# Kernel optimization log

Hardware: AMD Instinct MI355X
Metric: run time of the kernel (lower is better)

## Reference

```python
import jax, jax.numpy as jnp
import numpy as np

H = 32      # query heads
HK = 8      # kv heads
HD = 64     # head dim
D = 2048    # model dim
BASE = 10000.0
NEG = -1e9


def _rope_cos_sin(L):
    inv_freq = 1.0 / (BASE ** (jnp.arange(0, HD, 2, dtype=jnp.float32) / HD))  # [HD/2]
    freqs = jnp.arange(L, dtype=jnp.float32)[:, None] * inv_freq[None, :]       # [L, HD/2]
    emb = jnp.concatenate([freqs, freqs], axis=-1)                               # [L, HD]
    return jnp.cos(emb), jnp.sin(emb)


def _rotate_half(x):
    x1, x2 = jnp.split(x, 2, axis=-1)
    return jnp.concatenate([-x2, x1], axis=-1)


def setup_inputs() -> dict:
    key = jax.random.key(0)
    ks = jax.random.split(key, 5)
    B, L = 2, 2048
    x = jax.random.normal(ks[0], (B, L, D), dtype=jnp.float32)
    Wq = jax.random.normal(ks[1], (D, D), dtype=jnp.float32) * 0.02
    Wk = jax.random.normal(ks[2], (HK * HD, D), dtype=jnp.float32) * 0.02
    Wv = jax.random.normal(ks[3], (HK * HD, D), dtype=jnp.float32) * 0.02
    Wo = jax.random.normal(ks[4], (D, D), dtype=jnp.float32) * 0.02
    causal = jnp.where(jnp.tril(jnp.ones((L, L), dtype=bool)), 0.0, NEG)
    mask = causal[None, None].astype(jnp.float32)  # [1,1,L,L] additive mask
    return {"x": x, "Wq": Wq, "Wk": Wk, "Wv": Wv, "Wo": Wo, "mask": mask}


def reference(x, Wq, Wk, Wv, Wo, mask):
    B, L, _ = x.shape
    # projections (nn.Linear: y = x @ W^T), split heads -> [B, heads, L, HD]
    q = jnp.einsum('bld,ed->ble', x, Wq).reshape(B, L, H, HD).transpose(0, 2, 1, 3)
    k = jnp.einsum('bld,ed->ble', x, Wk).reshape(B, L, HK, HD).transpose(0, 2, 1, 3)
    v = jnp.einsum('bld,ed->ble', x, Wv).reshape(B, L, HK, HD).transpose(0, 2, 1, 3)
    # RoPE (plain branch: L <= original_max); cos/sin [L,HD] broadcast over B,heads
    cos, sin = _rope_cos_sin(L)
    q = q * cos + _rotate_half(q) * sin
    k = k * cos + _rotate_half(k) * sin
    # GQA: repeat_interleave kv heads to H heads
    rep = H // HK
    k = jnp.repeat(k, rep, axis=1)  # [B,H,L,HD]
    v = jnp.repeat(v, rep, axis=1)
    scores = jnp.einsum('bhld,bhmd->bhlm', q, k) / np.float32(np.sqrt(HD)) + mask
    attn = jax.nn.softmax(scores, axis=-1)
    out = jnp.einsum('bhlm,bhmd->blhd', attn, v).reshape(B, L, D)
    return jnp.einsum('ble,de->bld', out, Wo)
```

## Files before the change

kernel.cpp:

```cpp
#include <hip/hip_runtime.h>
#include <math.h>

#define NH 32
#define NHK 8
#define HD 64
#define DMODEL 2048
#define LSEQ 2048
#define NB 2
#define QKV_N 3072

typedef __attribute__((ext_vector_type(8))) short short8;
typedef __attribute__((ext_vector_type(4))) float floatx4;

__device__ __forceinline__ unsigned short f2bf(float f) {
  unsigned u = __float_as_uint(f);
  return (unsigned short)((u + 0x7FFFu + ((u >> 16) & 1u)) >> 16);
}
__device__ __forceinline__ float bf2f(unsigned short v) {
  return __uint_as_float((unsigned)v << 16);
}
__device__ __forceinline__ float fast_exp2(float x) {
#if __has_builtin(__builtin_amdgcn_exp2f)
  return __builtin_amdgcn_exp2f(x);
#else
  return __expf(x * 0.69314718f);
#endif
}
__device__ __forceinline__ unsigned pack_bf_trunc(float hi, float lo) {
  return __builtin_amdgcn_perm(__float_as_uint(hi), __float_as_uint(lo), 0x07060302u);
}
__device__ __forceinline__ void stage16g(const char* g_lane,
                                         unsigned short* lds_wave_base, int lane) {
#if __has_builtin(__builtin_amdgcn_global_load_lds)
  __builtin_amdgcn_global_load_lds(
      (const __attribute__((address_space(1))) void*)(g_lane),
      (__attribute__((address_space(3))) void*)(lds_wave_base), 16, 0, 0);
#else
  *(uint4*)(lds_wave_base + lane * 8) = *(const uint4*)g_lane;
#endif
}

__global__ __launch_bounds__(256) void rope_tab(float2* __restrict__ tab) {
  int i = blockIdx.x * 256 + threadIdx.x;
  int d = i & 31, l = i >> 5;
  float invf = (float)pow(10000.0, -(double)d / 32.0);
  float ang = (float)l * invf;
  double sd, cd;
  sincos((double)ang, &sd, &cd);
  tab[i] = make_float2((float)cd, (float)sd);
}

__global__ __launch_bounds__(256) void cvt_bf16(const float* __restrict__ src,
                                                unsigned short* __restrict__ dst,
                                                int n4) {
  int i = blockIdx.x * 256 + threadIdx.x;
  if (i >= n4) return;
  float4 v = ((const float4*)src)[i];
  ushort4 o;
  o.x = f2bf(v.x); o.y = f2bf(v.y); o.z = f2bf(v.z); o.w = f2bf(v.w);
  ((ushort4*)dst)[i] = o;
}

__global__ __launch_bounds__(256) void cvt_w3(const float* __restrict__ Wq,
                                              const float* __restrict__ Wk,
                                              const float* __restrict__ Wv,
                                              unsigned short* __restrict__ dst) {
  const int NQ = DMODEL * DMODEL / 4, NK = 512 * DMODEL / 4;
  int i = blockIdx.x * 256 + threadIdx.x;
  const float* src;
  int off;
  if (i < NQ) { src = Wq; off = i; }
  else if (i < NQ + NK) { src = Wk; off = i - NQ; }
  else { src = Wv; off = i - NQ - NK; }
  float4 v = ((const float4*)src)[off];
  ushort4 o;
  o.x = f2bf(v.x); o.y = f2bf(v.y); o.z = f2bf(v.z); o.w = f2bf(v.w);
  ((ushort4*)dst)[i] = o;
}

template <int BN, bool BF16C>
__global__ __launch_bounds__(512, 2) void gemm8(const unsigned short* __restrict__ A,
                                                const unsigned short* __restrict__ B,
                                                void* __restrict__ Cv, int K, int ldc) {
  constexpr int CN = BN / 64;
  constexpr int BUFB = BN * 32;
  __shared__ unsigned short As[4 * 256 * 32];
  __shared__ unsigned short Bs[4 * BUFB];

  const int tid = threadIdx.x;
  const int wave = tid >> 6, lane = tid & 63;
  const int quad = lane >> 4, l16 = lane & 15;
  const int wm = wave & 1, wn = wave >> 1;

  const int nwg = gridDim.x * gridDim.y;
  const int orig = blockIdx.y * gridDim.x + blockIdx.x;
  const int swz = (orig & 7) * (nwg >> 3) + (orig >> 3);
  const int bx = swz % gridDim.x, by = swz / gridDim.x;
  const int m0 = by * 256, n0 = bx * BN;

  const int kt = K >> 5;

  const int sgrow = wave * 16 + (lane >> 2);
  const int cchunk = (lane & 3) ^ ((lane >> 3) & 3);
  const char* AgB = (const char*)(A + (size_t)(m0 + sgrow) * K + cchunk * 8);
  const char* BgB = (const char*)(B + (size_t)(n0 + sgrow) * K + cchunk * 8);

  auto stageA = [&](int t2) {
    unsigned short* dst = &As[((t2 & 3) << 13) + wave * 512];
#pragma unroll
    for (int u = 0; u < 2; ++u)
      stage16g(AgB + ((size_t)u * 128 * K + (size_t)t2 * 32) * 2, dst + u * 4096, lane);
  };
  auto stageB = [&](int t2) {
    unsigned short* dst = &Bs[(t2 & 3) * BUFB + wave * 512];
#pragma unroll
    for (int u = 0; u < BN / 128; ++u)
      stage16g(BgB + ((size_t)u * 128 * K + (size_t)t2 * 32) * 2, dst + u * 4096, lane);
  };

  const int sw8 = (quad ^ ((l16 >> 1) & 3)) * 8;

  floatx4 acc[8][CN] = {};

  stageA(0); stageB(0);
  stageA(1); stageB(1);
  stageA(2); stageB(2);

#pragma unroll 1
  for (int t = 0; t < kt; ++t) {
    if (t + 2 < kt) {
      if constexpr (BN == 256) asm volatile("s_waitcnt vmcnt(8)" ::: "memory");
      else                     asm volatile("s_waitcnt vmcnt(6)" ::: "memory");
    } else if (t + 1 < kt) {
      if constexpr (BN == 256) asm volatile("s_waitcnt vmcnt(4)" ::: "memory");
      else                     asm volatile("s_waitcnt vmcnt(3)" ::: "memory");
    } else {
      asm volatile("s_waitcnt vmcnt(0)" ::: "memory");
    }
    __builtin_amdgcn_s_barrier();
    __builtin_amdgcn_sched_barrier(0);

    const unsigned short* Asb = &As[(t & 3) << 13];
    const unsigned short* Bsb = &Bs[(t & 3) * BUFB];
    const unsigned short* Arow = Asb + (wm * 128 + l16) * 32 + sw8;
    const unsigned short* Brow = Bsb + (wn * 16 * CN + l16) * 32 + sw8;

    short8 bfr[CN], af[4];
#pragma unroll
    for (int j = 0; j < CN; ++j) bfr[j] = *(const short8*)(Brow + j * 16 * 32);
#pragma unroll
    for (int i = 0; i < 4; ++i) af[i] = *(const short8*)(Arow + i * 16 * 32);

    if (t + 3 < kt) stageA(t + 3);

    __builtin_amdgcn_s_setprio(1);
#pragma unroll
    for (int i = 0; i < 4; ++i)
#pragma unroll
      for (int j = 0; j < CN; ++j)
        acc[i][j] = __builtin_amdgcn_mfma_f32_16x16x32_bf16(af[i], bfr[j], acc[i][j], 0, 0, 0);
    __builtin_amdgcn_s_setprio(0);

#pragma unroll
    for (int i = 0; i < 4; ++i) af[i] = *(const short8*)(Arow + (64 + i * 16) * 32);

    if (t + 3 < kt) stageB(t + 3);

    __builtin_amdgcn_s_setprio(1);
#pragma unroll
    for (int i = 0; i < 4; ++i)
#pragma unroll
      for (int j = 0; j < CN; ++j)
        acc[4 + i][j] = __builtin_amdgcn_mfma_f32_16x16x32_bf16(af[i], bfr[j], acc[4 + i][j], 0, 0, 0);
    __builtin_amdgcn_s_setprio(0);
  }

#pragma unroll
  for (int i = 0; i < 8; ++i)
#pragma unroll
    for (int j = 0; j < CN; ++j)
#pragma unroll
      for (int r = 0; r < 4; ++r) {
        size_t idx = (size_t)(m0 + wm * 128 + i * 16 + quad * 4 + r) * ldc +
                     n0 + wn * 16 * CN + j * 16 + l16;
        if (BF16C)
          ((unsigned short*)Cv)[idx] = f2bf(acc[i][j][r]);
        else
          ((float*)Cv)[idx] = acc[i][j][r];
      }
}

__global__ __launch_bounds__(256) void ropek_cvt2(const unsigned short* __restrict__ qkvb,
                                                  const float2* __restrict__ tab,
                                                  unsigned short* __restrict__ kb) {
  int t = blockIdx.x * 256 + threadIdx.x;
  int d = t & 31;
  int rest = t >> 5;
  int khead = rest & 7;
  int bl = rest >> 3;
  int l = bl & (LSEQ - 1);
  int b = bl >> 11;
  const unsigned short* src = qkvb + (size_t)bl * QKV_N + DMODEL + khead * HD;
  float2 cs = tab[(size_t)l * 32 + d];
  float x1 = bf2f(src[d]), x2 = bf2f(src[d + 32]);
  unsigned short* dst = kb + ((size_t)((b * NHK + khead) * LSEQ + l)) * HD;
  dst[d] = f2bf(x1 * cs.x - x2 * cs.y);
  dst[d + 32] = f2bf(x2 * cs.x + x1 * cs.y);
}

__global__ __launch_bounds__(256) void vt_cvt2(const unsigned short* __restrict__ qkvb,
                                               unsigned short* __restrict__ vtb) {
  __shared__ unsigned short Lt[64][72];
  const int tt = blockIdx.x, kh = blockIdx.y, b = blockIdx.z;
  const int tid = threadIdx.x;
  const unsigned short* src =
      qkvb + ((size_t)(b * LSEQ + tt * 64)) * QKV_N + DMODEL + 512 + kh * HD;
  {
    int row = tid >> 2, c0 = (tid & 3) * 16;
    *(uint4*)&Lt[row][c0] = *(const uint4*)(src + (size_t)row * QKV_N + c0);
    *(uint4*)&Lt[row][c0 + 8] = *(const uint4*)(src + (size_t)row * QKV_N + c0 + 8);
  }
  __syncthreads();
  {
    int d = tid >> 2, seg = tid & 3;
    unsigned short o[16];
#pragma unroll
    for (int k = 0; k < 16; ++k) o[k] = Lt[seg * 16 + k][d];
    unsigned short* dst =
        vtb + ((size_t)((b * NHK + kh) * 80 + d)) * LSEQ + tt * 64 + seg * 16;
    *(uint4*)dst = *(uint4*)o;
    *(uint4*)(dst + 8) = *(uint4*)(o + 8);
  }
  if (tid < 64)
    vtb[((size_t)((b * NHK + kh) * 80 + 64)) * LSEQ + tt * 64 + tid] = 0x3F80;
}

__global__ __launch_bounds__(256, 3) void attn8(const unsigned short* __restrict__ qkvb,
                                                const float2* __restrict__ tab,
                                                const unsigned short* __restrict__ kb,
                                                const unsigned short* __restrict__ vtb,
                                                unsigned short* __restrict__ out) {
  const int kh = blockIdx.x;
  const int p = 63 - blockIdx.y;
  const int b = blockIdx.z;
  const int wave = threadIdx.x >> 6, lane = threadIdx.x & 63;
  const int quad = lane >> 4, l16 = lane & 15;
  const int h = kh * 4 + wave;

  __shared__ unsigned short Kbuf[2][64 * 64];
  __shared__ unsigned short Vbuf[2][72 * 64];
  __shared__ unsigned short Ps_all[4][32][72];
  unsigned short(*Ps)[72] = Ps_all[wave];

  const char* kbaseB = (const char*)(kb + ((size_t)(b * NHK + kh) * LSEQ) * HD);
  const char* vbaseB = (const char*)(vtb + ((size_t)(b * NHK + kh) * 80) * LSEQ);
  const float QSCALE = 0.125f * 1.44269504f;

  short8 qf[2][2];
  floatx4 O[2][5];

  auto loadQ = [&](int qb) {
#pragma unroll
    for (int i = 0; i < 2; ++i) {
      const int tok = qb + i * 16 + l16;
      const unsigned short* qr =
          qkvb + ((size_t)(b * LSEQ + tok)) * QKV_N + h * HD + quad * 8;
      uint4 lo = *(const uint4*)qr;
      uint4 hi = *(const uint4*)(qr + 32);
      const float2* tr = tab + (size_t)tok * 32 + quad * 8;
      float4 cs01 = ((const float4*)tr)[0];
      float4 cs23 = ((const float4*)tr)[1];
      float4 cs45 = ((const float4*)tr)[2];
      float4 cs67 = ((const float4*)tr)[3];
      float cosv[8] = {cs01.x, cs01.z, cs23.x, cs23.z, cs45.x, cs45.z, cs67.x, cs67.z};
      float sinv[8] = {cs01.y, cs01.w, cs23.y, cs23.w, cs45.y, cs45.w, cs67.y, cs67.w};
      const unsigned short* plo = (const unsigned short*)&lo;
      const unsigned short* phi = (const unsigned short*)&hi;
      unsigned short olo[8], ohi[8];
#pragma unroll
      for (int j = 0; j < 8; ++j) {
        float x1 = bf2f(plo[j]), x2 = bf2f(phi[j]);
        olo[j] = f2bf((x1 * cosv[j] - x2 * sinv[j]) * QSCALE);
        ohi[j] = f2bf((x2 * cosv[j] + x1 * sinv[j]) * QSCALE);
      }
      qf[i][0] = *(const short8*)olo;
      qf[i][1] = *(const short8*)ohi;
    }
  };
  auto zeroO = [&]() {
#pragma unroll
    for (int i = 0; i < 2; ++i)
#pragma unroll
      for (int j = 0; j < 5; ++j) O[i][j] = (floatx4){0.f, 0.f, 0.f, 0.f};
  };
  auto epilogue = [&](int qb) {
#pragma unroll
    for (int i = 0; i < 2; ++i) {
      float lv = __shfl(O[i][4][0], l16);
      float inv = 1.0f / lv;
      const size_t obase =
          ((size_t)(b * LSEQ + qb + i * 16 + l16)) * DMODEL + h * HD;
#pragma unroll
      for (int j = 0; j < 4; ++j) {
        uint2 w;
        w.x = (unsigned)f2bf(O[i][j][0] * inv) | ((unsigned)f2bf(O[i][j][1] * inv) << 16);
        w.y = (unsigned)f2bf(O[i][j][2] * inv) | ((unsigned)f2bf(O[i][j][3] * inv) << 16);
        *(uint2*)&out[obase + j * 16 + quad * 4] = w;
      }
    }
  };
  auto stageKV = [&](int bi, int kt) {
    unsigned short* Kd = Kbuf[bi];
    unsigned short* Vd = Vbuf[bi];
#pragma unroll
    for (int c = wave; c < 17; c += 4) {
      if (c < 8) {
        int o = c * 1024 + lane * 16;
        int row = o >> 7;
        int lgc = ((o >> 4) & 7) ^ (row & 7);
        stage16g(kbaseB + (size_t)(kt * 64 + row) * 128 + lgc * 16,
                 Kd + c * 512, lane);
      } else {
        int o = (c - 8) * 1024 + lane * 16;
        int row = o >> 7;
        int lgc = ((o >> 4) & 7) ^ (row & 7);
        stage16g(vbaseB + (size_t)row * (LSEQ * 2) + (size_t)kt * 128 + lgc * 16,
                 Vd + (c - 8) * 512, lane);
      }
    }
  };

  const int qb = p * 32;
  const int last = p >> 1;
  const int N = last + 1;

  loadQ(qb);
  zeroO();
  stageKV(0, 0);

#pragma unroll 1
  for (int m = 0; m < N; ++m) {
    __syncthreads();

    if (m + 1 < N) stageKV((m + 1) & 1, m + 1);

    const int kt = m;
    const unsigned short* Ks = Kbuf[m & 1];
    const unsigned short* Vs = Vbuf[m & 1];

    short8 kf[4][2];
#pragma unroll
    for (int t = 0; t < 4; ++t)
#pragma unroll
      for (int hf = 0; hf < 2; ++hf) {
        int row = t * 16 + l16;
        int phys = (4 * hf + quad) ^ (row & 7);
        kf[t][hf] = *(const short8*)&Ks[row * 64 + phys * 8];
      }

    floatx4 st[4][2];
#pragma unroll
    for (int t = 0; t < 4; ++t)
#pragma unroll
      for (int i = 0; i < 2; ++i) {
        floatx4 z = {0.f, 0.f, 0.f, 0.f};
        z = __builtin_amdgcn_mfma_f32_16x16x32_bf16(kf[t][0], qf[i][0], z, 0, 0, 0);
        st[t][i] = __builtin_amdgcn_mfma_f32_16x16x32_bf16(kf[t][1], qf[i][1], z, 0, 0, 0);
      }

    if (kt == last) {
      const int kofs = kt * 64 - qb;
#pragma unroll
      for (int t = 0; t < 4; ++t) {
        const int krow = kofs + 16 * t + quad * 4;
#pragma unroll
        for (int i = 0; i < 2; ++i) {
          const int qcol = 16 * i + l16;
          float sv[4];
#pragma unroll
          for (int r = 0; r < 4; ++r) {
            float v = st[t][i][r];
            if (krow + r > qcol) v = -1e30f;
            sv[r] = fast_exp2(v);
          }
          uint2 w;
          w.x = pack_bf_trunc(sv[1], sv[0]);
          w.y = pack_bf_trunc(sv[3], sv[2]);
          *(uint2*)&Ps[16 * i + l16][16 * t + quad * 4] = w;
        }
      }
    } else {
#pragma unroll
      for (int t = 0; t < 4; ++t)
#pragma unroll
        for (int i = 0; i < 2; ++i) {
          float sv[4];
#pragma unroll
          for (int r = 0; r < 4; ++r) sv[r] = fast_exp2(st[t][i][r]);
          uint2 w;
          w.x = pack_bf_trunc(sv[1], sv[0]);
          w.y = pack_bf_trunc(sv[3], sv[2]);
          *(uint2*)&Ps[16 * i + l16][16 * t + quad * 4] = w;
        }
    }

    short8 pf[2][2];
#pragma unroll
    for (int i = 0; i < 2; ++i)
#pragma unroll
      for (int hh = 0; hh < 2; ++hh)
        pf[i][hh] = *(const short8*)&Ps[16 * i + l16][32 * hh + quad * 8];
#pragma unroll
    for (int j = 0; j < 5; ++j) {
      int row = (j == 4) ? (64 + (l16 & 7)) : (j * 16 + l16);
      short8 vf0 = *(const short8*)&Vs[row * 64 + ((quad ^ (row & 7)) * 8)];
      short8 vf1 = *(const short8*)&Vs[row * 64 + (((4 + quad) ^ (row & 7)) * 8)];
#pragma unroll
      for (int i = 0; i < 2; ++i) {
        O[i][j] = __builtin_amdgcn_mfma_f32_16x16x32_bf16(vf0, pf[i][0], O[i][j], 0, 0, 0);
        O[i][j] = __builtin_amdgcn_mfma_f32_16x16x32_bf16(vf1, pf[i][1], O[i][j], 0, 0, 0);
      }
    }
  }

  epilogue(qb);
}

extern "C" void kernel_launch(void* const* d_in, const int* in_sizes, int n_in,
                              void* d_out, int out_size, void* d_ws,
                              size_t ws_size, hipStream_t stream) {
  const float* x = (const float*)d_in[0];
  const float* Wq = (const float*)d_in[1];
  const float* Wk = (const float*)d_in[2];
  const float* Wv = (const float*)d_in[3];
  const float* Wo = (const float*)d_in[4];
  float* out = (float*)d_out;

  char* ws = (char*)d_ws;
  unsigned short* qkvb = (unsigned short*)ws;
  float2* tab = (float2*)(ws + 25165824);
  unsigned short* kbuf = (unsigned short*)(ws + 25690112);
  unsigned short* vtb = (unsigned short*)(ws + 29884416);
  unsigned short* xb = (unsigned short*)(ws + 35127296);
  unsigned short* wqkvb = (unsigned short*)(ws + 51904512);
  unsigned short* aob = xb;
  unsigned short* wob = wqkvb;

  const int M = NB * LSEQ;
  dim3 blk(256);

  rope_tab<<<(LSEQ * 32) / 256, blk, 0, stream>>>(tab);
  cvt_bf16<<<(M * DMODEL / 4 + 255) / 256, blk, 0, stream>>>(x, xb, M * DMODEL / 4);
  cvt_w3<<<(QKV_N * DMODEL / 4) / 256, blk, 0, stream>>>(Wq, Wk, Wv, wqkvb);

  gemm8<256, true><<<dim3(QKV_N / 256, M / 256), dim3(512), 0, stream>>>(
      xb, wqkvb, qkvb, DMODEL, QKV_N);

  ropek_cvt2<<<(NB * LSEQ * 8 * 32) / 256, blk, 0, stream>>>(qkvb, tab, kbuf);
  vt_cvt2<<<dim3(LSEQ / 64, NHK, NB), blk, 0, stream>>>(qkvb, vtb);

  attn8<<<dim3(NHK, 64, NB), blk, 0, stream>>>(qkvb, tab, kbuf, vtb, aob);

  cvt_bf16<<<(DMODEL * DMODEL / 4 + 255) / 256, blk, 0, stream>>>(Wo, wob, DMODEL * DMODEL / 4);

  gemm8<128, false><<<dim3(DMODEL / 128, M / 256), dim3(512), 0, stream>>>(
      aob, wob, out, DMODEL, DMODEL);
}
```

Measured before the change: 303.6 us.

## Merge prep and mid kernels, add phased barrier schedule to QKV GEMM

The RoPE table, x conversion and Wq/Wk/Wv conversion now run as a single prep kernel. K-RoPE, the V transpose and the Wo conversion are merged into a single mid kernel. Together these cut the launch count from nine to five and remove the small-kernel tail gaps. The QKV GEMM also gains a PHASED variant that adds workgroup barriers and lgkmcnt waits around each MFMA phase to keep waves in lockstep. Those extra barriers could cost stall time, and the mid kernel's shared-memory allocation now applies to every block.

```diff
diff --git a/kernel.cpp b/kernel.cpp
--- a/kernel.cpp
+++ b/kernel.cpp
@@ -40,45 +40,47 @@
 #endif
 }
 
-__global__ __launch_bounds__(256) void rope_tab(float2* __restrict__ tab) {
-  int i = blockIdx.x * 256 + threadIdx.x;
-  int d = i & 31, l = i >> 5;
-  float invf = (float)pow(10000.0, -(double)d / 32.0);
-  float ang = (float)l * invf;
-  double sd, cd;
-  sincos((double)ang, &sd, &cd);
-  tab[i] = make_float2((float)cd, (float)sd);
-}
-
-__global__ __launch_bounds__(256) void cvt_bf16(const float* __restrict__ src,
-                                                unsigned short* __restrict__ dst,
-                                                int n4) {
-  int i = blockIdx.x * 256 + threadIdx.x;
-  if (i >= n4) return;
-  float4 v = ((const float4*)src)[i];
-  ushort4 o;
-  o.x = f2bf(v.x); o.y = f2bf(v.y); o.z = f2bf(v.z); o.w = f2bf(v.w);
-  ((ushort4*)dst)[i] = o;
-}
-
-__global__ __launch_bounds__(256) void cvt_w3(const float* __restrict__ Wq,
-                                              const float* __restrict__ Wk,
-                                              const float* __restrict__ Wv,
-                                              unsigned short* __restrict__ dst) {
+__global__ __launch_bounds__(256) void prep(const float* __restrict__ x,
+                                            const float* __restrict__ Wq,
+                                            const float* __restrict__ Wk,
+                                            const float* __restrict__ Wv,
+                                            float2* __restrict__ tab,
+                                            unsigned short* __restrict__ xb,
+                                            unsigned short* __restrict__ wqkvb) {
+  const int NTAB = LSEQ * 32;
+  const int NX = NB * LSEQ * DMODEL / 4;
+  int idx = blockIdx.x * 256 + threadIdx.x;
+  if (idx < NTAB) {
+    int d = idx & 31, l = idx >> 5;
+    float invf = (float)pow(10000.0, -(double)d / 32.0);
+    float ang = (float)l * invf;
+    double sd, cd;
+    sincos((double)ang, &sd, &cd);
+    tab[idx] = make_float2((float)cd, (float)sd);
+    return;
+  }
+  idx -= NTAB;
+  if (idx < NX) {
+    float4 v = ((const float4*)x)[idx];
+    ushort4 o;
+    o.x = f2bf(v.x); o.y = f2bf(v.y); o.z = f2bf(v.z); o.w = f2bf(v.w);
+    ((ushort4*)xb)[idx] = o;
+    return;
+  }
+  idx -= NX;
   const int NQ = DMODEL * DMODEL / 4, NK = 512 * DMODEL / 4;
-  int i = blockIdx.x * 256 + threadIdx.x;
   const float* src;
   int off;
-  if (i < NQ) { src = Wq; off = i; }
-  else if (i < NQ + NK) { src = Wk; off = i - NQ; }
-  else { src = Wv; off = i - NQ - NK; }
+  if (idx < NQ) { src = Wq; off = idx; }
+  else if (idx < NQ + NK) { src = Wk; off = idx - NQ; }
+  else { src = Wv; off = idx - NQ - NK; }
   float4 v = ((const float4*)src)[off];
   ushort4 o;
   o.x = f2bf(v.x); o.y = f2bf(v.y); o.z = f2bf(v.z); o.w = f2bf(v.w);
-  ((ushort4*)dst)[i] = o;
-}
-
-template <int BN, bool BF16C>
+  ((ushort4*)wqkvb)[idx] = o;
+}
+
+template <int BN, bool BF16C, bool PHASED>
 __global__ __launch_bounds__(512, 2) void gemm8(const unsigned short* __restrict__ A,
                                                 const unsigned short* __restrict__ B,
                                                 void* __restrict__ Cv, int K, int ldc) {
@@ -146,33 +148,71 @@
     const unsigned short* Brow = Bsb + (wn * 16 * CN + l16) * 32 + sw8;
 
     short8 bfr[CN], af[4];
-#pragma unroll
-    for (int j = 0; j < CN; ++j) bfr[j] = *(const short8*)(Brow + j * 16 * 32);
-#pragma unroll
-    for (int i = 0; i < 4; ++i) af[i] = *(const short8*)(Arow + i * 16 * 32);
-
-    if (t + 3 < kt) stageA(t + 3);
-
-    __builtin_amdgcn_s_setprio(1);
-#pragma unroll
-    for (int i = 0; i < 4; ++i)
-#pragma unroll
-      for (int j = 0; j < CN; ++j)
-        acc[i][j] = __builtin_amdgcn_mfma_f32_16x16x32_bf16(af[i], bfr[j], acc[i][j], 0, 0, 0);
-    __builtin_amdgcn_s_setprio(0);
-
-#pragma unroll
-    for (int i = 0; i < 4; ++i) af[i] = *(const short8*)(Arow + (64 + i * 16) * 32);
-
-    if (t + 3 < kt) stageB(t + 3);
-
-    __builtin_amdgcn_s_setprio(1);
-#pragma unroll
-    for (int i = 0; i < 4; ++i)
-#pragma unroll
-      for (int j = 0; j < CN; ++j)
-        acc[4 + i][j] = __builtin_amdgcn_mfma_f32_16x16x32_bf16(af[i], bfr[j], acc[4 + i][j], 0, 0, 0);
-    __builtin_amdgcn_s_setprio(0);
+
+    if constexpr (PHASED) {
+#pragma unroll
+      for (int j = 0; j < CN; ++j) bfr[j] = *(const short8*)(Brow + j * 16 * 32);
+#pragma unroll
+      for (int i = 0; i < 4; ++i) af[i] = *(const short8*)(Arow + i * 16 * 32);
+      if (t + 3 < kt) stageA(t + 3);
+
+      __builtin_amdgcn_s_barrier();
+      asm volatile("s_waitcnt lgkmcnt(0)" ::: "memory");
+      __builtin_amdgcn_sched_barrier(0);
+      __builtin_amdgcn_s_setprio(1);
+#pragma unroll
+      for (int i = 0; i < 4; ++i)
+#pragma unroll
+        for (int j = 0; j < CN; ++j)
+          acc[i][j] = __builtin_amdgcn_mfma_f32_16x16x32_bf16(af[i], bfr[j], acc[i][j], 0, 0, 0);
+      __builtin_amdgcn_s_setprio(0);
+      __builtin_amdgcn_sched_barrier(0);
+      __builtin_amdgcn_s_barrier();
+
+#pragma unroll
+      for (int i = 0; i < 4; ++i) af[i] = *(const short8*)(Arow + (64 + i * 16) * 32);
+      if (t + 3 < kt) stageB(t + 3);
+
+      __builtin_amdgcn_s_barrier();
+      asm volatile("s_waitcnt lgkmcnt(0)" ::: "memory");
+      __builtin_amdgcn_sched_barrier(0);
+      __builtin_amdgcn_s_setprio(1);
+#pragma unroll
+      for (int i = 0; i < 4; ++i)
+#pragma unroll
+        for (int j = 0; j < CN; ++j)
+          acc[4 + i][j] = __builtin_amdgcn_mfma_f32_16x16x32_bf16(af[i], bfr[j], acc[4 + i][j], 0, 0, 0);
+      __builtin_amdgcn_s_setprio(0);
+      __builtin_amdgcn_sched_barrier(0);
+    } else {
+#pragma unroll
+      for (int j = 0; j < CN; ++j) bfr[j] = *(const short8*)(Brow + j * 16 * 32);
+#pragma unroll
+      for (int i = 0; i < 4; ++i) af[i] = *(const short8*)(Arow + i * 16 * 32);
+
+      if (t + 3 < kt) stageA(t + 3);
+
+      __builtin_amdgcn_s_setprio(1);
+#pragma unroll
+      for (int i = 0; i < 4; ++i)
+#pragma unroll
+        for (int j = 0; j < CN; ++j)
+          acc[i][j] = __builtin_amdgcn_mfma_f32_16x16x32_bf16(af[i], bfr[j], acc[i][j], 0, 0, 0);
+      __builtin_amdgcn_s_setprio(0);
+
+#pragma unroll
+      for (int i = 0; i < 4; ++i) af[i] = *(const short8*)(Arow + (64 + i * 16) * 32);
+
+      if (t + 3 < kt) stageB(t + 3);
+
+      __builtin_amdgcn_s_setprio(1);
+#pragma unroll
+      for (int i = 0; i < 4; ++i)
+#pragma unroll
+        for (int j = 0; j < CN; ++j)
+          acc[4 + i][j] = __builtin_amdgcn_mfma_f32_16x16x32_bf16(af[i], bfr[j], acc[4 + i][j], 0, 0, 0);
+      __builtin_amdgcn_s_setprio(0);
+    }
   }
 
 #pragma unroll
@@ -190,49 +230,58 @@
       }
 }
 
-__global__ __launch_bounds__(256) void ropek_cvt2(const unsigned short* __restrict__ qkvb,
-                                                  const float2* __restrict__ tab,
-                                                  unsigned short* __restrict__ kb) {
-  int t = blockIdx.x * 256 + threadIdx.x;
-  int d = t & 31;
-  int rest = t >> 5;
-  int khead = rest & 7;
-  int bl = rest >> 3;
-  int l = bl & (LSEQ - 1);
-  int b = bl >> 11;
-  const unsigned short* src = qkvb + (size_t)bl * QKV_N + DMODEL + khead * HD;
-  float2 cs = tab[(size_t)l * 32 + d];
-  float x1 = bf2f(src[d]), x2 = bf2f(src[d + 32]);
-  unsigned short* dst = kb + ((size_t)((b * NHK + khead) * LSEQ + l)) * HD;
-  dst[d] = f2bf(x1 * cs.x - x2 * cs.y);
-  dst[d + 32] = f2bf(x2 * cs.x + x1 * cs.y);
-}
-
-__global__ __launch_bounds__(256) void vt_cvt2(const unsigned short* __restrict__ qkvb,
-                                               unsigned short* __restrict__ vtb) {
+__global__ __launch_bounds__(256) void mid(const unsigned short* __restrict__ qkvb,
+                                           const float2* __restrict__ tab,
+                                           const float* __restrict__ Wo,
+                                           unsigned short* __restrict__ kb,
+                                           unsigned short* __restrict__ vtb,
+                                           unsigned short* __restrict__ wob) {
   __shared__ unsigned short Lt[64][72];
-  const int tt = blockIdx.x, kh = blockIdx.y, b = blockIdx.z;
-  const int tid = threadIdx.x;
-  const unsigned short* src =
-      qkvb + ((size_t)(b * LSEQ + tt * 64)) * QKV_N + DMODEL + 512 + kh * HD;
-  {
-    int row = tid >> 2, c0 = (tid & 3) * 16;
-    *(uint4*)&Lt[row][c0] = *(const uint4*)(src + (size_t)row * QKV_N + c0);
-    *(uint4*)&Lt[row][c0 + 8] = *(const uint4*)(src + (size_t)row * QKV_N + c0 + 8);
+  const int bid = blockIdx.x, tid = threadIdx.x;
+  if (bid < 4096) {
+    int t = bid * 256 + tid;
+    int d = t & 31;
+    int rest = t >> 5;
+    int khead = rest & 7;
+    int bl = rest >> 3;
+    int l = bl & (LSEQ - 1);
+    int b = bl >> 11;
+    const unsigned short* src = qkvb + (size_t)bl * QKV_N + DMODEL + khead * HD;
+    float2 cs = tab[(size_t)l * 32 + d];
+    float x1 = bf2f(src[d]), x2 = bf2f(src[d + 32]);
+    unsigned short* dst = kb + ((size_t)((b * NHK + khead) * LSEQ + l)) * HD;
+    dst[d] = f2bf(x1 * cs.x - x2 * cs.y);
+    dst[d + 32] = f2bf(x2 * cs.x + x1 * cs.y);
+  } else if (bid < 4608) {
+    const int vtid = bid - 4096;
+    const int tt = vtid & 31, kh = (vtid >> 5) & 7, b = vtid >> 8;
+    const unsigned short* src =
+        qkvb + ((size_t)(b * LSEQ + tt * 64)) * QKV_N + DMODEL + 512 + kh * HD;
+    {
+      int row = tid >> 2, c0 = (tid & 3) * 16;
+      *(uint4*)&Lt[row][c0] = *(const uint4*)(src + (size_t)row * QKV_N + c0);
+      *(uint4*)&Lt[row][c0 + 8] = *(const uint4*)(src + (size_t)row * QKV_N + c0 + 8);
+    }
+    __syncthreads();
+    {
+      int d = tid >> 2, seg = tid & 3;
+      unsigned short o[16];
+#pragma unroll
+      for (int k = 0; k < 16; ++k) o[k] = Lt[seg * 16 + k][d];
+      unsigned short* dst =
+          vtb + ((size_t)((b * NHK + kh) * 80 + d)) * LSEQ + tt * 64 + seg * 16;
+      *(uint4*)dst = *(uint4*)o;
+      *(uint4*)(dst + 8) = *(uint4*)(o + 8);
+    }
+    if (tid < 64)
+      vtb[((size_t)((b * NHK + kh) * 80 + 64)) * LSEQ + tt * 64 + tid] = 0x3F80;
+  } else {
+    int i = (bid - 4608) * 256 + tid;
+    float4 v = ((const float4*)Wo)[i];
+    ushort4 o;
+    o.x = f2bf(v.x); o.y = f2bf(v.y); o.z = f2bf(v.z); o.w = f2bf(v.w);
+    ((ushort4*)wob)[i] = o;
   }
-  __syncthreads();
-  {
-    int d = tid >> 2, seg = tid & 3;
-    unsigned short o[16];
-#pragma unroll
-    for (int k = 0; k < 16; ++k) o[k] = Lt[seg * 16 + k][d];
-    unsigned short* dst =
-        vtb + ((size_t)((b * NHK + kh) * 80 + d)) * LSEQ + tt * 64 + seg * 16;
-    *(uint4*)dst = *(uint4*)o;
-    *(uint4*)(dst + 8) = *(uint4*)(o + 8);
-  }
-  if (tid < 64)
-    vtb[((size_t)((b * NHK + kh) * 80 + 64)) * LSEQ + tt * 64 + tid] = 0x3F80;
 }
 
 __global__ __launch_bounds__(256, 3) void attn8(const unsigned short* __restrict__ qkvb,
@@ -449,20 +498,15 @@
   const int M = NB * LSEQ;
   dim3 blk(256);
 
-  rope_tab<<<(LSEQ * 32) / 256, blk, 0, stream>>>(tab);
-  cvt_bf16<<<(M * DMODEL / 4 + 255) / 256, blk, 0, stream>>>(x, xb, M * DMODEL / 4);
-  cvt_w3<<<(QKV_N * DMODEL / 4) / 256, blk, 0, stream>>>(Wq, Wk, Wv, wqkvb);
-
-  gemm8<256, true><<<dim3(QKV_N / 256, M / 256), dim3(512), 0, stream>>>(
+  prep<<<14592, blk, 0, stream>>>(x, Wq, Wk, Wv, tab, xb, wqkvb);
+
+  gemm8<256, true, true><<<dim3(QKV_N / 256, M / 256), dim3(512), 0, stream>>>(
       xb, wqkvb, qkvb, DMODEL, QKV_N);
 
-  ropek_cvt2<<<(NB * LSEQ * 8 * 32) / 256, blk, 0, stream>>>(qkvb, tab, kbuf);
-  vt_cvt2<<<dim3(LSEQ / 64, NHK, NB), blk, 0, stream>>>(qkvb, vtb);
+  mid<<<8704, blk, 0, stream>>>(qkvb, tab, Wo, kbuf, vtb, wob);
 
   attn8<<<dim3(NHK, 64, NB), blk, 0, stream>>>(qkvb, tab, kbuf, vtb, aob);
 
-  cvt_bf16<<<(DMODEL * DMODEL / 4 + 255) / 256, blk, 0, stream>>>(Wo, wob, DMODEL * DMODEL / 4);
-
-  gemm8<128, false><<<dim3(DMODEL / 128, M / 256), dim3(512), 0, stream>>>(
+  gemm8<128, false, false><<<dim3(DMODEL / 128, M / 256), dim3(512), 0, stream>>>(
       aob, wob, out, DMODEL, DMODEL);
 }
```

Result: no change. 299.1 us (-1.5%).
